# Optimization experiments

Measured on AMD Instinct MI355X. Metric: run time of the kernel, lower is better.

## Reference

```python
import jax, jax.numpy as jnp
import numpy as np

B, R, D = 64, 4, 768
H = W = 37
ROI_SIDE = 5


def setup_inputs() -> dict:
    key = jax.random.key(0)
    k1, k2, k3 = jax.random.split(key, 3)
    return {
        "cls_tok": jax.random.normal(k1, (B, D), dtype=jnp.float32),
        "regs": jax.random.normal(k2, (B, R, D), dtype=jnp.float32),
        "patches2d": jax.random.normal(k3, (B, H, W, D), dtype=jnp.float32),
        "roi_side": ROI_SIDE,
    }


def reference(cls_tok, regs, patches2d, roi_side):
    # cues: [B, C, d] with C = 1 + n_registers
    cues = jnp.concatenate([cls_tok[:, None, :], regs], axis=1)
    b, h_dim, w_dim, d = patches2d.shape
    r = roi_side // 2

    # similarity of every cue against every patch: [B, C, H, W]
    sim = jnp.einsum('bcd,bhwd->bchw', cues, patches2d)
    idx = jnp.argmax(sim.reshape(b, cues.shape[1], h_dim * w_dim), axis=-1)  # [B, C]
    hh = idx // w_dim
    ww = idx % w_dim

    # clipped window slice [max(0,h-r), min(H,h+r+1)) == rows with |row-h| <= r
    rows = jnp.arange(h_dim)
    cols = jnp.arange(w_dim)
    rmask = jnp.abs(rows[None, None, :] - hh[:, :, None]) <= r  # [B, C, H]
    cmask = jnp.abs(cols[None, None, :] - ww[:, :, None]) <= r  # [B, C, W]
    mask = (rmask[:, :, :, None] & cmask[:, :, None, :]).astype(patches2d.dtype)  # [B,C,H,W]

    num = jnp.einsum('bchw,bhwd->bcd', mask, patches2d)
    cnt = jnp.sum(mask, axis=(2, 3))  # [B, C]
    rois = num / cnt[:, :, None]      # mean over the (clipped) ROI window

    toks = jnp.concatenate([cues, rois], axis=1)  # [B, 2C, d]
    nrm = jnp.maximum(jnp.linalg.norm(toks, axis=-1, keepdims=True), 1e-12)
    return toks / nrm
```

## Files before the change

kernel.cpp:

```cpp
#include <hip/hip_runtime.h>
#include <hip/hip_bf16.h>

#define NB   64
#define NREG 4
#define ND   768
#define NH   37
#define NW   37
#define NC   5
#define NP   (NH * NW)
#define BPB  16
#define PPB  ((NP + BPB - 1) / BPB)
#define NWAVE 4
#define DEPTH 2

__device__ __forceinline__ unsigned int ord_of(float f) {
    unsigned int u = __float_as_uint(f);
    return (u & 0x80000000u) ? ~u : (u | 0x80000000u);
}

template <int CTRL>
__device__ __forceinline__ float dpp_add_step(float x) {
    int y = __builtin_amdgcn_update_dpp(0, __float_as_int(x), CTRL, 0xf, 0xf, true);
    return x + __int_as_float(y);
}
__device__ __forceinline__ float wave_sum_lane63(float x) {
    x = dpp_add_step<0x111>(x);
    x = dpp_add_step<0x112>(x);
    x = dpp_add_step<0x114>(x);
    x = dpp_add_step<0x118>(x);
    x = dpp_add_step<0x142>(x);
    x = dpp_add_step<0x143>(x);
    return x;
}

__device__ __forceinline__ void stage_patch(const float* __restrict__ gbase,
                                            float* lslot, int lane) {
    const float* g = gbase + lane * 4;
    #pragma unroll
    for (int k = 0; k < 3; ++k) {
        __builtin_amdgcn_global_load_lds(
            (const __attribute__((address_space(1))) void*)(g + k * 256),
            (__attribute__((address_space(3))) void*)(lslot + k * 256),
            16, 0, 0);
    }
}

__global__ __launch_bounds__(256, 4) void sim_argmax_kernel(
    const float* __restrict__ cls_tok,
    const float* __restrict__ regs,
    const float* __restrict__ patches,
    unsigned long long* __restrict__ pkeys)
{
    const int b    = blockIdx.x / BPB;
    const int pb   = blockIdx.x % BPB;
    const int wave = threadIdx.x >> 6;
    const int lane = threadIdx.x & 63;

    __shared__ float lds[DEPTH][NWAVE][ND];

    float4 cue[NC][3];
    #pragma unroll
    for (int c = 0; c < NC; ++c) {
        const float* cb = (c == 0) ? (cls_tok + (size_t)b * ND)
                                   : (regs + ((size_t)b * NREG + (c - 1)) * ND);
        #pragma unroll
        for (int k = 0; k < 3; ++k)
            cue[c][k] = *reinterpret_cast<const float4*>(cb + k * 256 + lane * 4);
    }

    float best[NC];
    int   bidx[NC];
    #pragma unroll
    for (int c = 0; c < NC; ++c) { best[c] = -3.4e38f; bidx[c] = 0; }

    const int pstart = pb * PPB;
    const int p1     = min(NP, pstart + PPB);
    const size_t bb  = (size_t)b * NP;
    const int p0     = pstart + wave;

    #pragma unroll
    for (int s = 0; s < DEPTH; ++s) {
        const int pp = p0 + s * NWAVE;
        if (pp < p1) stage_patch(patches + (bb + pp) * ND, &lds[s][wave][0], lane);
    }

    int it = 0;
    for (int pp = p0; pp < p1; pp += NWAVE, ++it) {
        const int s = it & 1;
        const bool more = (pp + NWAVE) < p1;

        if (more) asm volatile("s_waitcnt vmcnt(3)" ::: "memory");
        else      asm volatile("s_waitcnt vmcnt(0)" ::: "memory");

        const float* l = &lds[s][wave][0] + lane * 4;
        const float4 v0 = *reinterpret_cast<const float4*>(l);
        const float4 v1 = *reinterpret_cast<const float4*>(l + 256);
        const float4 v2 = *reinterpret_cast<const float4*>(l + 512);

        asm volatile("s_waitcnt lgkmcnt(0)" ::: "memory");

        const int pf = pp + DEPTH * NWAVE;
        if (pf < p1) stage_patch(patches + (bb + pf) * ND, &lds[s][wave][0], lane);

        float sacc[NC];
        #pragma unroll
        for (int c = 0; c < NC; ++c) {
            sacc[c] = v0.x * cue[c][0].x + v0.y * cue[c][0].y
                    + v0.z * cue[c][0].z + v0.w * cue[c][0].w
                    + v1.x * cue[c][1].x + v1.y * cue[c][1].y
                    + v1.z * cue[c][1].z + v1.w * cue[c][1].w
                    + v2.x * cue[c][2].x + v2.y * cue[c][2].y
                    + v2.z * cue[c][2].z + v2.w * cue[c][2].w;
        }
        #pragma unroll
        for (int c = 0; c < NC; ++c) {
            const float t = wave_sum_lane63(sacc[c]);
            if (t > best[c]) { best[c] = t; bidx[c] = pp; }
        }
    }

    __shared__ unsigned long long lk[NWAVE][NC];
    if (lane == 63) {
        #pragma unroll
        for (int c = 0; c < NC; ++c) {
            lk[wave][c] =
                ((unsigned long long)ord_of(best[c]) << 32) |
                (unsigned long long)(unsigned)(NP - 1 - bidx[c]);
        }
    }
    __syncthreads();
    if (threadIdx.x < NC) {
        unsigned long long k = lk[0][threadIdx.x];
        k = max(k, lk[1][threadIdx.x]);
        k = max(k, lk[2][threadIdx.x]);
        k = max(k, lk[3][threadIdx.x]);
        pkeys[(b * NC + threadIdx.x) * BPB + pb] = k;
    }
}

__global__ __launch_bounds__(256) void roi_norm_kernel(
    const float* __restrict__ cls_tok,
    const float* __restrict__ regs,
    const float* __restrict__ patches,
    const unsigned long long* __restrict__ pkeys,
    const int* __restrict__ roi_side_p,
    float* __restrict__ out)
{
    const int b   = blockIdx.x / NC;
    const int c   = blockIdx.x % NC;
    const int tid = threadIdx.x;
    const int wave = tid >> 6, lane = tid & 63;
    const int r = roi_side_p[0] >> 1;

    const unsigned long long* pk = pkeys + (b * NC + c) * BPB;
    unsigned long long key = pk[0];
    #pragma unroll
    for (int i = 1; i < BPB; ++i) key = max(key, pk[i]);

    const int idx = NP - 1 - (int)(key & 0xFFFFFFFFu);
    const int hh = idx / NW, ww = idx % NW;
    const int h0 = max(0, hh - r), h1 = min(NH - 1, hh + r);
    const int w0 = max(0, ww - r), w1 = min(NW - 1, ww + r);
    const float inv_cnt = 1.0f / (float)((h1 - h0 + 1) * (w1 - w0 + 1));

    float a0 = 0.f, a1 = 0.f, a2 = 0.f;
    for (int h = h0; h <= h1; ++h) {
        for (int w = w0; w <= w1; ++w) {
            const float* p = patches + ((size_t)b * NP + h * NW + w) * ND;
            a0 += p[tid];
            a1 += p[tid + 256];
            a2 += p[tid + 512];
        }
    }
    a0 *= inv_cnt; a1 *= inv_cnt; a2 *= inv_cnt;

    const float* cb = (c == 0) ? (cls_tok + (size_t)b * ND)
                               : (regs + ((size_t)b * NREG + (c - 1)) * ND);
    const float v0 = cb[tid], v1 = cb[tid + 256], v2 = cb[tid + 512];

    float sx = v0 * v0 + v1 * v1 + v2 * v2;
    float sy = a0 * a0 + a1 * a1 + a2 * a2;
    #pragma unroll
    for (int off = 32; off > 0; off >>= 1) {
        sx += __shfl_xor(sx, off, 64);
        sy += __shfl_xor(sy, off, 64);
    }
    __shared__ float red_x[4], red_y[4];
    if (lane == 0) { red_x[wave] = sx; red_y[wave] = sy; }
    __syncthreads();
    const float tot_x = red_x[0] + red_x[1] + red_x[2] + red_x[3];
    const float tot_y = red_y[0] + red_y[1] + red_y[2] + red_y[3];
    const float inv_nc = 1.0f / fmaxf(sqrtf(tot_x), 1e-12f);
    const float inv_nr = 1.0f / fmaxf(sqrtf(tot_y), 1e-12f);

    float* oc = out + ((size_t)b * 2 * NC + c) * ND;
    float* om = out + ((size_t)b * 2 * NC + NC + c) * ND;
    oc[tid]       = v0 * inv_nc;
    oc[tid + 256] = v1 * inv_nc;
    oc[tid + 512] = v2 * inv_nc;
    om[tid]       = a0 * inv_nr;
    om[tid + 256] = a1 * inv_nr;
    om[tid + 512] = a2 * inv_nr;
}

extern "C" void kernel_launch(void* const* d_in, const int* in_sizes, int n_in,
                              void* d_out, int out_size, void* d_ws, size_t ws_size,
                              hipStream_t stream) {
    const float* cls_tok = (const float*)d_in[0];
    const float* regs    = (const float*)d_in[1];
    const float* patches = (const float*)d_in[2];
    const int*   roi     = (const int*)d_in[3];
    float* out = (float*)d_out;
    unsigned long long* pkeys = (unsigned long long*)d_ws;

    sim_argmax_kernel<<<NB * BPB, 256, 0, stream>>>(cls_tok, regs, patches, pkeys);
    roi_norm_kernel<<<NB * NC, 256, 0, stream>>>(cls_tok, regs, patches, pkeys, roi, out);
}
```

Before: 57.47 us.

## Replace LDS-staged patch pipeline with 5-deep register prefetch ring

Removes the global_load_lds staging buffer and manual waitcnt scheme. Each wave now prefetches patch rows straight into a 5-slot register ring, using an unrolled body that reloads a slot once its dot products are done. Blocks per batch drop from 16 to 12 and the occupancy hint goes from 4 to 3 to make room for the extra registers. This is meant to keep more loads in flight and skip the LDS round trip, at the cost of higher register pressure, fewer waves and fewer blocks.

```diff
diff --git a/kernel.cpp b/kernel.cpp
--- a/kernel.cpp
+++ b/kernel.cpp
@@ -8,10 +8,10 @@
 #define NW   37
 #define NC   5
 #define NP   (NH * NW)
-#define BPB  16
+#define BPB  12
 #define PPB  ((NP + BPB - 1) / BPB)
 #define NWAVE 4
-#define DEPTH 2
+#define DEPTH 5
 
 __device__ __forceinline__ unsigned int ord_of(float f) {
     unsigned int u = __float_as_uint(f);
@@ -33,19 +33,7 @@
     return x;
 }
 
-__device__ __forceinline__ void stage_patch(const float* __restrict__ gbase,
-                                            float* lslot, int lane) {
-    const float* g = gbase + lane * 4;
-    #pragma unroll
-    for (int k = 0; k < 3; ++k) {
-        __builtin_amdgcn_global_load_lds(
-            (const __attribute__((address_space(1))) void*)(g + k * 256),
-            (__attribute__((address_space(3))) void*)(lslot + k * 256),
-            16, 0, 0);
-    }
-}
-
-__global__ __launch_bounds__(256, 4) void sim_argmax_kernel(
+__global__ __launch_bounds__(256, 3) void sim_argmax_kernel(
     const float* __restrict__ cls_tok,
     const float* __restrict__ regs,
     const float* __restrict__ patches,
@@ -56,8 +44,6 @@
     const int wave = threadIdx.x >> 6;
     const int lane = threadIdx.x & 63;
 
-    __shared__ float lds[DEPTH][NWAVE][ND];
-
     float4 cue[NC][3];
     #pragma unroll
     for (int c = 0; c < NC; ++c) {
@@ -76,48 +62,62 @@
     const int pstart = pb * PPB;
     const int p1     = min(NP, pstart + PPB);
     const size_t bb  = (size_t)b * NP;
-    const int p0     = pstart + wave;
-
-    #pragma unroll
-    for (int s = 0; s < DEPTH; ++s) {
-        const int pp = p0 + s * NWAVE;
-        if (pp < p1) stage_patch(patches + (bb + pp) * ND, &lds[s][wave][0], lane);
-    }
-
-    int it = 0;
-    for (int pp = p0; pp < p1; pp += NWAVE, ++it) {
-        const int s = it & 1;
-        const bool more = (pp + NWAVE) < p1;
-
-        if (more) asm volatile("s_waitcnt vmcnt(3)" ::: "memory");
-        else      asm volatile("s_waitcnt vmcnt(0)" ::: "memory");
-
-        const float* l = &lds[s][wave][0] + lane * 4;
-        const float4 v0 = *reinterpret_cast<const float4*>(l);
-        const float4 v1 = *reinterpret_cast<const float4*>(l + 256);
-        const float4 v2 = *reinterpret_cast<const float4*>(l + 512);
-
-        asm volatile("s_waitcnt lgkmcnt(0)" ::: "memory");
-
-        const int pf = pp + DEPTH * NWAVE;
-        if (pf < p1) stage_patch(patches + (bb + pf) * ND, &lds[s][wave][0], lane);
-
-        float sacc[NC];
-        #pragma unroll
-        for (int c = 0; c < NC; ++c) {
-            sacc[c] = v0.x * cue[c][0].x + v0.y * cue[c][0].y
-                    + v0.z * cue[c][0].z + v0.w * cue[c][0].w
-                    + v1.x * cue[c][1].x + v1.y * cue[c][1].y
-                    + v1.z * cue[c][1].z + v1.w * cue[c][1].w
-                    + v2.x * cue[c][2].x + v2.y * cue[c][2].y
-                    + v2.z * cue[c][2].z + v2.w * cue[c][2].w;
+    int p = pstart + wave;
+
+#define LOAD_SLOT(Sa, Sb, Sc, pp)                                              \
+    {                                                                          \
+        const float* g_ = patches + (bb + (pp)) * ND + lane * 4;               \
+        Sa = *reinterpret_cast<const float4*>(g_);                             \
+        Sb = *reinterpret_cast<const float4*>(g_ + 256);                       \
+        Sc = *reinterpret_cast<const float4*>(g_ + 512);                       \
+    }
+
+    float4 S0a, S0b, S0c, S1a, S1b, S1c, S2a, S2b, S2c,
+           S3a, S3b, S3c, S4a, S4b, S4c;
+    const float4 z = make_float4(0.f, 0.f, 0.f, 0.f);
+    S0a=S0b=S0c=S1a=S1b=S1c=S2a=S2b=S2c=S3a=S3b=S3c=S4a=S4b=S4c=z;
+
+    if (p + 0*NWAVE < p1) LOAD_SLOT(S0a, S0b, S0c, p + 0*NWAVE);
+    if (p + 1*NWAVE < p1) LOAD_SLOT(S1a, S1b, S1c, p + 1*NWAVE);
+    if (p + 2*NWAVE < p1) LOAD_SLOT(S2a, S2b, S2c, p + 2*NWAVE);
+    if (p + 3*NWAVE < p1) LOAD_SLOT(S3a, S3b, S3c, p + 3*NWAVE);
+    if (p + 4*NWAVE < p1) LOAD_SLOT(S4a, S4b, S4c, p + 4*NWAVE);
+
+#define BODY(Sa, Sb, Sc)                                                       \
+    {                                                                          \
+        float s_[NC];                                                          \
+        _Pragma("unroll")                                                      \
+        for (int c = 0; c < NC; ++c) {                                         \
+            s_[c] = Sa.x * cue[c][0].x + Sa.y * cue[c][0].y                    \
+                  + Sa.z * cue[c][0].z + Sa.w * cue[c][0].w                    \
+                  + Sb.x * cue[c][1].x + Sb.y * cue[c][1].y                    \
+                  + Sb.z * cue[c][1].z + Sb.w * cue[c][1].w                    \
+                  + Sc.x * cue[c][2].x + Sc.y * cue[c][2].y                    \
+                  + Sc.z * cue[c][2].z + Sc.w * cue[c][2].w;                   \
+        }                                                                      \
+        const int pf_ = p + DEPTH * NWAVE;                                     \
+        if (pf_ < p1) LOAD_SLOT(Sa, Sb, Sc, pf_);                              \
+        _Pragma("unroll")                                                      \
+        for (int c = 0; c < NC; ++c) {                                         \
+            const float t_ = wave_sum_lane63(s_[c]);                           \
+            if (t_ > best[c]) { best[c] = t_; bidx[c] = p; }                   \
+        }                                                                      \
+        p += NWAVE;                                                            \
+        if (p >= p1) goto done;                                                \
+    }
+
+    if (p < p1) {
+        while (true) {
+            BODY(S0a, S0b, S0c)
+            BODY(S1a, S1b, S1c)
+            BODY(S2a, S2b, S2c)
+            BODY(S3a, S3b, S3c)
+            BODY(S4a, S4b, S4c)
         }
-        #pragma unroll
-        for (int c = 0; c < NC; ++c) {
-            const float t = wave_sum_lane63(sacc[c]);
-            if (t > best[c]) { best[c] = t; bidx[c] = pp; }
-        }
-    }
+    }
+done: ;
+#undef BODY
+#undef LOAD_SLOT
 
     __shared__ unsigned long long lk[NWAVE][NC];
     if (lane == 63) {
```

After: 97.46 us. 1.7x slower.
